# Kernel optimization log

Hardware: AMD Instinct MI355X
Metric: run time of the kernel (lower is better)

Reference implementation:

```python
import jax, jax.numpy as jnp
import numpy as np

CONF_T = 0.05
IOU_T = 0.5
K_PER_CLASS = 200  # max_detections_per_class
MAX_DET = 200      # max_detections
VAR = jnp.array([0.1, 0.1, 0.2, 0.2], jnp.float32)


def setup_inputs() -> dict:
    key = jax.random.key(0)
    k1, k2, k3, k4 = jax.random.split(key, 4)
    B, A, C = 8, 76725, 80
    # logits shifted down so most sigmoid scores fall below threshold (realistic)
    head_classifier = jax.random.normal(k1, (B, A, C), jnp.float32) - 2.0
    head_regression = jax.random.normal(k2, (B, A, 4), jnp.float32)
    centers = jax.random.uniform(k3, (A, 2), jnp.float32, 0.0, 640.0)
    sizes = jax.random.uniform(k4, (A, 2), jnp.float32, 16.0, 256.0)
    anchor_boxes = jnp.concatenate([centers, sizes], axis=-1)  # (cx, cy, w, h)
    return {"head_classifier": head_classifier,
            "head_regression": head_regression,
            "anchor_boxes": anchor_boxes}


def _decode(anchors, box_pred):
    # anchors: [1, A, 4] (cx,cy,w,h); box_pred: [B, A, 4]
    b = box_pred * VAR
    cxcy = b[..., :2] * anchors[..., 2:] + anchors[..., :2]
    wh = jnp.exp(b[..., 2:]) * anchors[..., 2:]
    # center -> corner coordinates (x1, y1, x2, y2)
    return jnp.concatenate([cxcy - wh * 0.5, cxcy + wh * 0.5], axis=-1)


def _pairwise_iou(bx):
    # bx: [K, 4] corner boxes -> [K, K] IoU
    x1, y1, x2, y2 = jnp.split(bx, 4, axis=-1)  # each [K, 1]
    area = jnp.squeeze((x2 - x1) * (y2 - y1), -1)  # [K]
    ix1 = jnp.maximum(x1, x1.T)
    iy1 = jnp.maximum(y1, y1.T)
    ix2 = jnp.minimum(x2, x2.T)
    iy2 = jnp.minimum(y2, y2.T)
    inter = jnp.clip(ix2 - ix1, 0.0) * jnp.clip(iy2 - iy1, 0.0)  # [K, K]
    union = area[:, None] + area[None, :] - inter
    return inter / jnp.maximum(union, 1e-8)


def _nms_one_class(scores, boxes):
    # scores: [A], boxes: [A, 4] -> top-K greedy NMS
    vals, idx = jax.lax.top_k(scores, K_PER_CLASS)
    b = boxes[idx]  # [K, 4]
    valid = vals > CONF_T
    iou = _pairwise_iou(b)  # [K, K]
    order = jnp.arange(K_PER_CLASS)

    def body(i, keep):
        # if box i is kept, suppress later boxes overlapping it above IOU_T
        sup = (iou[i] > IOU_T) & (order > i) & keep[i]
        return keep & ~sup

    keep = jax.lax.fori_loop(0, K_PER_CLASS, body, valid)
    return jnp.where(keep, vals, -1.0), b


def _combined(cls_scores, boxes):
    # cls_scores: [A, C], boxes: [A, 4] (shared across classes, q=1)
    sc, bx = jax.vmap(lambda s: _nms_one_class(s, boxes), in_axes=1)(cls_scores)
    C = sc.shape[0]
    cls_ids = jnp.broadcast_to(
        jnp.arange(C, dtype=jnp.float32)[:, None], (C, K_PER_CLASS))
    sc_f = sc.reshape(-1)          # [C*K]
    bx_f = bx.reshape(-1, 4)       # [C*K, 4]
    cl_f = cls_ids.reshape(-1)     # [C*K]
    top_v, top_i = jax.lax.top_k(sc_f, MAX_DET)
    ok = top_v > 0.0  # surviving detections (kept scores exceed CONF_T > 0)
    nmsed_boxes = jnp.where(ok[:, None], bx_f[top_i], 0.0)
    nmsed_scores = jnp.where(ok, top_v, 0.0)
    nmsed_classes = jnp.where(ok, cl_f[top_i], 0.0)
    valid = jnp.sum(ok).astype(jnp.int32)
    return nmsed_boxes, nmsed_scores, nmsed_classes, valid


def reference(head_classifier, head_regression, anchor_boxes):
    cls_predictions = jax.nn.sigmoid(head_classifier)          # [B, A, C]
    boxes = _decode(anchor_boxes[None, ...], head_regression)  # [B, A, 4]
    return jax.vmap(_combined)(cls_predictions, boxes)
```

## Files before the change

### kernel.cpp

```cpp
#include <hip/hip_runtime.h>
#include <cstdint>

#define TPB 256

constexpr int B_ = 8;
constexpr int A_ = 76725;
constexpr int C_ = 80;
constexpr int K_ = 200;
constexpr int S_ = 16;
constexpr int CAPS = 96;
constexpr int NBC = B_ * C_;
constexpr int P_ = 16;
constexpr int SL_ = C_ * K_ / P_;
constexpr float T0 = 0.4f;
constexpr float CONF_Tf = 0.05f;
constexpr float IOU_Tf = 0.5f;

__device__ inline uint64_t pack_key(float v, unsigned idx) {
  unsigned u = __float_as_uint(v);
  u = (u & 0x80000000u) ? ~u : (u | 0x80000000u);
  return ((uint64_t)u << 32) | (uint64_t)(0xFFFFFFFFu ^ idx);
}
__device__ inline float key_val(uint64_t k) {
  unsigned u = (unsigned)(k >> 32);
  u = (u & 0x80000000u) ? (u & 0x7FFFFFFFu) : ~u;
  return __uint_as_float(u);
}
__device__ inline unsigned key_idx(uint64_t k) { return 0xFFFFFFFFu ^ (unsigned)k; }

__device__ void radix_select(uint64_t* act, uint64_t* nxt, int n, int R,
                             uint64_t* sel, int* scnt, unsigned* hist,
                             int* s_d, int* s_ncnt) {
  int tid = threadIdx.x;
  if (tid == 0) *scnt = 0;
  __syncthreads();
  if (n <= R) {
    for (int i = tid; i < n; i += TPB) sel[i] = act[i];
    if (tid == 0) *scnt = n;
    __syncthreads();
    return;
  }
  int w = tid >> 6;
  for (int shift = 56; shift >= 0; shift -= 8) {
    for (int i = tid; i < 4 * 256; i += TPB) hist[i] = 0;
    __syncthreads();
    for (int i = tid; i < n; i += TPB)
      atomicAdd(&hist[(w << 8) + (int)((act[i] >> shift) & 255)], 1u);
    __syncthreads();
    if (tid < 256)
      hist[tid] = hist[tid] + hist[256 + tid] + hist[512 + tid] + hist[768 + tid];
    __syncthreads();
    for (int off = 1; off < 256; off <<= 1) {
      unsigned add = (tid < 256 && tid + off < 256) ? hist[tid + off] : 0u;
      __syncthreads();
      if (tid < 256) hist[tid] += add;
      __syncthreads();
    }
    if (tid < 256) {
      unsigned s = hist[tid];
      unsigned s1 = (tid == 255) ? 0u : hist[tid + 1];
      if ((int)s >= R && (int)s1 < R) *s_d = tid;
    }
    if (tid == 0) *s_ncnt = 0;
    __syncthreads();
    int d = *s_d;
    int above = (d == 255) ? 0 : (int)hist[d + 1];
    int cntd = (int)hist[d] - above;
    int need = R - above;
    if (need == cntd) {
      for (int i = tid; i < n; i += TPB)
        if ((int)((act[i] >> shift) & 255) >= d) sel[atomicAdd(scnt, 1)] = act[i];
      __syncthreads();
      return;
    }
    if (cntd == n) { R = need; continue; }
    for (int i = tid; i < n; i += TPB) {
      int dg = (int)((act[i] >> shift) & 255);
      if (dg > d) sel[atomicAdd(scnt, 1)] = act[i];
      else if (dg == d) nxt[atomicAdd(s_ncnt, 1)] = act[i];
    }
    __syncthreads();
    uint64_t* t = act; act = nxt; nxt = t;
    n = cntd; R = need;
  }
  for (int i = tid; i < R && i < n; i += TPB) sel[atomicAdd(scnt, 1)] = act[i];
  __syncthreads();
}

__device__ inline uint64_t shfl_xor_u64(uint64_t x, int m) {
  unsigned lo = (unsigned)__shfl_xor((int)(unsigned)x, m, 64);
  unsigned hi = (unsigned)__shfl_xor((int)(x >> 32), m, 64);
  return ((uint64_t)hi << 32) | lo;
}
__device__ void sort256_desc(uint64_t* sel) {
  int tid = threadIdx.x;
  uint64_t v = sel[tid];
  for (int k = 2; k <= 256; k <<= 1) {
    for (int j = k >> 1; j > 0; j >>= 1) {
      uint64_t other;
      if (j >= 64) {
        sel[tid] = v;
        __syncthreads();
        other = sel[tid ^ j];
        __syncthreads();
      } else {
        other = shfl_xor_u64(v, j);
      }
      bool up = ((tid & k) == 0);
      bool lower = ((tid & j) == 0);
      bool takeMax = (up == lower);
      bool sw = takeMax ? (other > v) : (other < v);
      v = sw ? other : v;
    }
  }
  sel[tid] = v;
  __syncthreads();
}

__device__ inline void bitonic_sort_desc_1024(uint64_t* buf, int tid) {
  for (int k = 2; k <= 1024; k <<= 1) {
    for (int j = k >> 1; j > 0; j >>= 1) {
      for (int i = tid; i < 1024; i += TPB) {
        int ixj = i ^ j;
        if (ixj > i) {
          uint64_t a = buf[i], b = buf[ixj];
          bool dir = ((i & k) == 0);
          if ((a < b) == dir) { buf[i] = b; buf[ixj] = a; }
        }
      }
      __syncthreads();
    }
  }
}
__device__ inline void compact_topk(uint64_t* buf, int* s_cnt, float* s_thr, int tid) {
  int cnt = *s_cnt;
  if (cnt > 1024) cnt = 1024;
  for (int i = cnt + tid; i < 1024; i += TPB) buf[i] = 0;
  __syncthreads();
  bitonic_sort_desc_1024(buf, tid);
  if (tid == 0) {
    *s_cnt = cnt < K_ ? cnt : K_;
    if (cnt >= K_) *s_thr = key_val(buf[K_ - 1]);
  }
  __syncthreads();
}
template <typename F>
__device__ inline void stream_topk(int n, F fetch, uint64_t* buf, int* s_cnt,
                                   float* s_thr, int tid) {
  for (int base = 0; base < n; base += TPB) {
    int i = base + tid;
    if (i < n) {
      uint64_t key; float v;
      fetch(i, key, v);
      if (v >= *s_thr) {
        int p = atomicAdd(s_cnt, 1);
        if (p < 1024) buf[p] = key;
      }
    }
    __syncthreads();
    int cur = *s_cnt;
    __syncthreads();
    if (cur >= 768) compact_topk(buf, s_cnt, s_thr, tid);
  }
  compact_topk(buf, s_cnt, s_thr, tid);
}

__global__ __launch_bounds__(TPB) void decode_kernel(const float4* __restrict__ regs,
                                                     const float4* __restrict__ anchors,
                                                     float4* __restrict__ boxes) {
  int idx = blockIdx.x * TPB + threadIdx.x;
  if (idx >= B_ * A_) return;
  int a = idx % A_;
  float4 r = regs[idx];
  float4 an = anchors[a];
  float bx = __fmul_rn(r.x, 0.1f), by = __fmul_rn(r.y, 0.1f);
  float bw = __fmul_rn(r.z, 0.2f), bh = __fmul_rn(r.w, 0.2f);
  float cx = __fadd_rn(__fmul_rn(bx, an.z), an.x);
  float cy = __fadd_rn(__fmul_rn(by, an.w), an.y);
  float w  = __fmul_rn(expf(bw), an.z);
  float h  = __fmul_rn(expf(bh), an.w);
  float hw = __fmul_rn(w, 0.5f), hh = __fmul_rn(h, 0.5f);
  boxes[idx] = make_float4(__fsub_rn(cx, hw), __fsub_rn(cy, hh),
                           __fadd_rn(cx, hw), __fadd_rn(cy, hh));
}

__global__ __launch_bounds__(TPB) void candidates_kernel(const float* __restrict__ logits,
                                                         uint64_t* __restrict__ lists,
                                                         int* __restrict__ cnts) {
  constexpr int ANCH = 256;
  constexpr int nT = (A_ + ANCH - 1) / ANCH;
  int bb = blockIdx.x / nT, t = blockIdx.x - bb * nT;
  int a0 = t * ANCH;
  int na = min(ANCH, A_ - a0);
  int bucket = blockIdx.x & (S_ - 1);
  const float4* src = (const float4*)(logits + ((size_t)bb * A_ + (size_t)a0) * C_);
  const int nq = na * (C_ / 4);
  for (int q0 = threadIdx.x; q0 < nq; q0 += TPB * 4) {
    float4 v[4];
    int qv[4] = {q0, q0 + TPB, q0 + 2 * TPB, q0 + 3 * TPB};
#pragma unroll
    for (int u = 0; u < 4; ++u)
      if (qv[u] < nq) v[u] = src[qv[u]];
#pragma unroll
    for (int u = 0; u < 4; ++u) {
      int q = qv[u];
      if (q >= nq) continue;
      float lv[4] = {v[u].x, v[u].y, v[u].z, v[u].w};
      int pos = q * 4;
      int al = pos / C_;
      int c  = pos - al * C_;
#pragma unroll
      for (int j = 0; j < 4; ++j) {
        float l = lv[j];
        if (l > T0) {
          float s = 1.0f / (1.0f + expf(-l));
          int cc = bb * C_ + c + j;
          int p = atomicAdd(&cnts[(cc * S_ + bucket) * 16], 1);
          if (p < CAPS)
            lists[((size_t)cc * S_ + bucket) * CAPS + p] = pack_key(s, (unsigned)(a0 + al));
        }
      }
    }
  }
}

__global__ __launch_bounds__(TPB) void class_nms_kernel(const float* __restrict__ logits,
                                                        const float4* __restrict__ boxes,
                                                        const uint64_t* __restrict__ lists,
                                                        const int* __restrict__ cnts,
                                                        float* __restrict__ cls_scores,
                                                        unsigned* __restrict__ cls_aidx) {
  __shared__ uint64_t s_bufA[1024];
  __shared__ uint64_t s_bufB[1024];
  __shared__ uint64_t s_sel[256];
  __shared__ unsigned s_hist[4 * 256];
  __shared__ int s_scnt, s_d, s_ncnt;
  __shared__ int s_off[S_ + 1];
  __shared__ int s_ok;
  __shared__ int s_cnt;
  __shared__ float s_thr;
  __shared__ float4 s_box[K_];
  __shared__ float s_score[K_], s_area[K_];
  __shared__ unsigned s_aidx[K_];
  __shared__ unsigned long long s_mask[K_][4];
  __shared__ unsigned long long s_keep[4];

  int tid = threadIdx.x;
  int cc = blockIdx.x;
  int bb = cc / C_, c = cc - bb * C_;

  if (tid == 0) {
    int acc = 0, ok = 1;
    for (int s = 0; s < S_; ++s) {
      int cn = cnts[(cc * S_ + s) * 16];
      if (cn > CAPS) { ok = 0; cn = CAPS; }
      s_off[s] = acc; acc += cn;
    }
    s_off[S_] = acc;
    s_ok = ok && (acc >= K_) && (acc <= 1024);
    s_cnt = 0; s_thr = CONF_Tf;
  }
  __syncthreads();
  int total = s_off[S_];
  int m;

  if (s_ok) {
    for (int s = 0; s < S_; ++s) {
      int n = s_off[s + 1] - s_off[s];
      const uint64_t* lp = lists + ((size_t)cc * S_ + s) * CAPS;
      for (int j = tid; j < n; j += TPB) s_bufA[s_off[s] + j] = lp[j];
    }
    __syncthreads();
    radix_select(s_bufA, s_bufB, total, K_, s_sel, &s_scnt, s_hist, &s_d, &s_ncnt);
    m = s_scnt;
    if (tid >= m) s_sel[tid] = 0;
    __syncthreads();
    sort256_desc(s_sel);
  } else {
    const float* col = logits + (size_t)bb * A_ * C_ + c;
    stream_topk(A_,
        [&](int i, uint64_t& key, float& v) {
          float l = col[(size_t)i * C_];
          v = 1.0f / (1.0f + expf(-l));
          key = pack_key(v, (unsigned)i);
        },
        s_bufA, &s_cnt, &s_thr, tid);
    m = s_cnt;
    s_sel[tid] = (tid < m) ? s_bufA[tid] : 0;
    __syncthreads();
  }

  if (tid < K_) {
    if (tid < m) {
      uint64_t key = s_sel[tid];
      unsigned a = key_idx(key);
      float sc = key_val(key);
      float4 bx = boxes[(size_t)bb * A_ + a];
      s_score[tid] = sc; s_aidx[tid] = a; s_box[tid] = bx;
      s_area[tid] = __fmul_rn(__fsub_rn(bx.z, bx.x), __fsub_rn(bx.w, bx.y));
    } else {
      s_score[tid] = -1.0f; s_aidx[tid] = 0u;
      s_box[tid] = make_float4(0.f, 0.f, 0.f, 0.f); s_area[tid] = 0.f;
    }
  }
  __syncthreads();

  if (tid < K_) {
    float4 bk = s_box[tid];
    float ak = s_area[tid];
    unsigned long long mw[4] = {0ull, 0ull, 0ull, 0ull};
    for (int i = 0; i < tid; ++i) {
      float4 bi = s_box[i];
      float ix1 = fmaxf(bk.x, bi.x), iy1 = fmaxf(bk.y, bi.y);
      float ix2 = fminf(bk.z, bi.z), iy2 = fminf(bk.w, bi.w);
      float iw = fmaxf(__fsub_rn(ix2, ix1), 0.f);
      float ih = fmaxf(__fsub_rn(iy2, iy1), 0.f);
      float inter = __fmul_rn(iw, ih);
      float uni = __fsub_rn(__fadd_rn(ak, s_area[i]), inter);
      float iou = inter / fmaxf(uni, 1e-8f);
      if (iou > IOU_Tf) mw[i >> 6] |= (1ull << (i & 63));
    }
    s_mask[tid][0] = mw[0]; s_mask[tid][1] = mw[1];
    s_mask[tid][2] = mw[2]; s_mask[tid][3] = mw[3];
  }
  __syncthreads();

  if (tid == 0) {
    unsigned long long k0 = 0, k1 = 0, k2 = 0, k3 = 0;
    for (int i = 0; i < m; ++i) {
      if (s_score[i] > CONF_Tf) {
        bool sup = ((s_mask[i][0] & k0) | (s_mask[i][1] & k1) |
                    (s_mask[i][2] & k2) | (s_mask[i][3] & k3)) != 0ull;
        if (!sup) {
          if (i < 64)       k0 |= 1ull << i;
          else if (i < 128) k1 |= 1ull << (i - 64);
          else if (i < 192) k2 |= 1ull << (i - 128);
          else              k3 |= 1ull << (i - 192);
        }
      }
    }
    s_keep[0] = k0; s_keep[1] = k1; s_keep[2] = k2; s_keep[3] = k3;
  }
  __syncthreads();

  if (tid < K_) {
    bool kept = (tid < m) && ((s_keep[tid >> 6] >> (tid & 63)) & 1ull);
    size_t o = (size_t)cc * K_ + tid;
    cls_scores[o] = kept ? s_score[tid] : -1.0f;
    cls_aidx[o] = s_aidx[tid];
  }
}

__global__ __launch_bounds__(TPB) void part_topk_kernel(const float* __restrict__ cls_scores,
                                                        uint64_t* __restrict__ tmp) {
  __shared__ uint64_t bufA[SL_];
  __shared__ uint64_t bufB[SL_];
  __shared__ uint64_t sel[256];
  __shared__ unsigned hist[4 * 256];
  __shared__ int s_scnt, s_d, s_ncnt;
  int tid = threadIdx.x;
  int bb = blockIdx.x / P_, part = blockIdx.x - bb * P_;
  int f0 = part * SL_;
  const float* sc = cls_scores + (size_t)bb * C_ * K_ + f0;
  for (int i = tid; i < SL_; i += TPB) bufA[i] = pack_key(sc[i], (unsigned)(f0 + i));
  __syncthreads();
  radix_select(bufA, bufB, SL_, K_, sel, &s_scnt, hist, &s_d, &s_ncnt);
  if (tid < K_) tmp[(size_t)blockIdx.x * K_ + tid] = sel[tid];
}

__global__ __launch_bounds__(TPB) void final_topk_kernel(const float4* __restrict__ boxes,
                                                         const uint64_t* __restrict__ tmp,
                                                         const unsigned* __restrict__ cls_aidx,
                                                         float* __restrict__ out) {
  constexpr int NF = P_ * K_;
  __shared__ uint64_t bufA[NF];
  __shared__ uint64_t bufB[NF];
  __shared__ uint64_t sel[256];
  __shared__ unsigned hist[4 * 256];
  __shared__ int s_scnt, s_d, s_ncnt, s_m;
  int tid = threadIdx.x;
  int bb = blockIdx.x;
  const uint64_t* tp = tmp + (size_t)bb * NF;
  for (int i = tid; i < NF; i += TPB) bufA[i] = tp[i];
  __syncthreads();
  radix_select(bufA, bufB, NF, K_, sel, &s_scnt, hist, &s_d, &s_ncnt);
  if (tid >= s_scnt) sel[tid] = 0;
  if (tid == 0) s_m = K_;
  __syncthreads();
  sort256_desc(sel);
  if (tid < K_) {
    float v = key_val(sel[tid]);
    if (!(v > 0.0f)) atomicMin(&s_m, tid);
  }
  __syncthreads();
  int m = s_m;

  if (tid < K_) {
    float4 bx = make_float4(0.f, 0.f, 0.f, 0.f);
    float sv = 0.f, cv = 0.f;
    if (tid < m) {
      uint64_t key = sel[tid];
      unsigned f = key_idx(key);
      sv = key_val(key);
      cv = (float)(f / K_);
      unsigned a = cls_aidx[(size_t)bb * C_ * K_ + f];
      bx = boxes[(size_t)bb * A_ + a];
    }
    ((float4*)out)[(size_t)bb * K_ + tid] = bx;
    out[B_ * K_ * 4 + bb * K_ + tid] = sv;
    out[B_ * K_ * 5 + bb * K_ + tid] = cv;
  }
  if (tid == 0) out[B_ * K_ * 6 + bb] = (float)m;
}

extern "C" void kernel_launch(void* const* d_in, const int* in_sizes, int n_in,
                              void* d_out, int out_size, void* d_ws, size_t ws_size,
                              hipStream_t stream) {
  const float* logits  = (const float*)d_in[0];
  const float4* regs   = (const float4*)d_in[1];
  const float4* anchors = (const float4*)d_in[2];
  float* out = (float*)d_out;

  char* ws = (char*)d_ws;
  float4* boxes     = (float4*)ws;                 size_t off = (size_t)B_ * A_ * 16;
  uint64_t* lists   = (uint64_t*)(ws + off);       off += (size_t)NBC * S_ * CAPS * 8;
  int* cnts         = (int*)(ws + off);            off += (size_t)NBC * S_ * 16 * 4;
  float* cls_scores = (float*)(ws + off);          off += (size_t)NBC * K_ * 4;
  unsigned* cls_aidx = (unsigned*)(ws + off);      off += (size_t)NBC * K_ * 4;
  uint64_t* tmp     = (uint64_t*)(ws + off);

  hipMemsetAsync(cnts, 0, (size_t)NBC * S_ * 16 * 4, stream);
  decode_kernel<<<(B_ * A_ + TPB - 1) / TPB, TPB, 0, stream>>>(regs, anchors, boxes);
  constexpr int nT = (A_ + 255) / 256;
  candidates_kernel<<<B_ * nT, TPB, 0, stream>>>(logits, lists, cnts);
  class_nms_kernel<<<NBC, TPB, 0, stream>>>(logits, boxes, lists, cnts,
                                            cls_scores, cls_aidx);
  part_topk_kernel<<<B_ * P_, TPB, 0, stream>>>(cls_scores, tmp);
  final_topk_kernel<<<B_, TPB, 0, stream>>>(boxes, tmp, cls_aidx, out);
}
```

Before: 443.5 us.

## Fuse box decode into NMS and aggregate candidates in shared memory per block

Removes the standalone decode kernel and decodes boxes only for the top-K selected anchors inside the class NMS kernel. Each class then stores its boxes directly, so the final kernel no longer gathers through anchor indices. The candidate kernel now buffers per-class hits in shared memory before one global atomic per class, and uses a single flat list of up to 1024 entries per class instead of 16 striped buckets. This cuts the full-size box workspace traffic and global atomic contention. In exchange it adds shared-memory pressure in the candidate kernel, and the unordered single list may change which overflow entries are dropped.

```diff
diff --git a/kernel.cpp b/kernel.cpp
--- a/kernel.cpp
+++ b/kernel.cpp
@@ -7,8 +7,8 @@
 constexpr int A_ = 76725;
 constexpr int C_ = 80;
 constexpr int K_ = 200;
-constexpr int S_ = 16;
-constexpr int CAPS = 96;
+constexpr int CAP = 1024;
+constexpr int LCAP = 16;
 constexpr int NBC = B_ * C_;
 constexpr int P_ = 16;
 constexpr int SL_ = C_ * K_ / P_;
@@ -165,37 +165,23 @@
   compact_topk(buf, s_cnt, s_thr, tid);
 }
 
-__global__ __launch_bounds__(TPB) void decode_kernel(const float4* __restrict__ regs,
-                                                     const float4* __restrict__ anchors,
-                                                     float4* __restrict__ boxes) {
-  int idx = blockIdx.x * TPB + threadIdx.x;
-  if (idx >= B_ * A_) return;
-  int a = idx % A_;
-  float4 r = regs[idx];
-  float4 an = anchors[a];
-  float bx = __fmul_rn(r.x, 0.1f), by = __fmul_rn(r.y, 0.1f);
-  float bw = __fmul_rn(r.z, 0.2f), bh = __fmul_rn(r.w, 0.2f);
-  float cx = __fadd_rn(__fmul_rn(bx, an.z), an.x);
-  float cy = __fadd_rn(__fmul_rn(by, an.w), an.y);
-  float w  = __fmul_rn(expf(bw), an.z);
-  float h  = __fmul_rn(expf(bh), an.w);
-  float hw = __fmul_rn(w, 0.5f), hh = __fmul_rn(h, 0.5f);
-  boxes[idx] = make_float4(__fsub_rn(cx, hw), __fsub_rn(cy, hh),
-                           __fadd_rn(cx, hw), __fadd_rn(cy, hh));
-}
-
 __global__ __launch_bounds__(TPB) void candidates_kernel(const float* __restrict__ logits,
                                                          uint64_t* __restrict__ lists,
                                                          int* __restrict__ cnts) {
+  __shared__ uint64_t s_cand[C_][LCAP];
+  __shared__ int s_cnt[C_];
   constexpr int ANCH = 256;
   constexpr int nT = (A_ + ANCH - 1) / ANCH;
   int bb = blockIdx.x / nT, t = blockIdx.x - bb * nT;
   int a0 = t * ANCH;
   int na = min(ANCH, A_ - a0);
-  int bucket = blockIdx.x & (S_ - 1);
+  int tid = threadIdx.x;
+  for (int c = tid; c < C_; c += TPB) s_cnt[c] = 0;
+  __syncthreads();
+
   const float4* src = (const float4*)(logits + ((size_t)bb * A_ + (size_t)a0) * C_);
   const int nq = na * (C_ / 4);
-  for (int q0 = threadIdx.x; q0 < nq; q0 += TPB * 4) {
+  for (int q0 = tid; q0 < nq; q0 += TPB * 4) {
     float4 v[4];
     int qv[4] = {q0, q0 + TPB, q0 + 2 * TPB, q0 + 3 * TPB};
 #pragma unroll
@@ -214,69 +200,72 @@
         float l = lv[j];
         if (l > T0) {
           float s = 1.0f / (1.0f + expf(-l));
-          int cc = bb * C_ + c + j;
-          int p = atomicAdd(&cnts[(cc * S_ + bucket) * 16], 1);
-          if (p < CAPS)
-            lists[((size_t)cc * S_ + bucket) * CAPS + p] = pack_key(s, (unsigned)(a0 + al));
+          uint64_t key = pack_key(s, (unsigned)(a0 + al));
+          int p = atomicAdd(&s_cnt[c + j], 1);
+          if (p < LCAP) {
+            s_cand[c + j][p] = key;
+          } else {
+            int cc = bb * C_ + c + j;
+            int g = atomicAdd(&cnts[cc * 16], 1);
+            if (g < CAP) lists[(size_t)cc * CAP + g] = key;
+          }
         }
       }
     }
   }
+  __syncthreads();
+
+  if (tid < C_) {
+    int n = min(s_cnt[tid], LCAP);
+    if (n > 0) {
+      int cc = bb * C_ + tid;
+      int base = atomicAdd(&cnts[cc * 16], n);
+      uint64_t* dst = lists + (size_t)cc * CAP;
+      for (int j = 0; j < n; ++j) {
+        int p = base + j;
+        if (p < CAP) dst[p] = s_cand[tid][j];
+      }
+    }
+  }
 }
 
 __global__ __launch_bounds__(TPB) void class_nms_kernel(const float* __restrict__ logits,
-                                                        const float4* __restrict__ boxes,
+                                                        const float4* __restrict__ regs,
+                                                        const float4* __restrict__ anchors,
                                                         const uint64_t* __restrict__ lists,
                                                         const int* __restrict__ cnts,
                                                         float* __restrict__ cls_scores,
-                                                        unsigned* __restrict__ cls_aidx) {
+                                                        float4* __restrict__ cls_boxes) {
   __shared__ uint64_t s_bufA[1024];
   __shared__ uint64_t s_bufB[1024];
   __shared__ uint64_t s_sel[256];
   __shared__ unsigned s_hist[4 * 256];
   __shared__ int s_scnt, s_d, s_ncnt;
-  __shared__ int s_off[S_ + 1];
-  __shared__ int s_ok;
   __shared__ int s_cnt;
   __shared__ float s_thr;
   __shared__ float4 s_box[K_];
   __shared__ float s_score[K_], s_area[K_];
-  __shared__ unsigned s_aidx[K_];
   __shared__ unsigned long long s_mask[K_][4];
   __shared__ unsigned long long s_keep[4];
 
   int tid = threadIdx.x;
   int cc = blockIdx.x;
   int bb = cc / C_, c = cc - bb * C_;
-
-  if (tid == 0) {
-    int acc = 0, ok = 1;
-    for (int s = 0; s < S_; ++s) {
-      int cn = cnts[(cc * S_ + s) * 16];
-      if (cn > CAPS) { ok = 0; cn = CAPS; }
-      s_off[s] = acc; acc += cn;
-    }
-    s_off[S_] = acc;
-    s_ok = ok && (acc >= K_) && (acc <= 1024);
-    s_cnt = 0; s_thr = CONF_Tf;
-  }
-  __syncthreads();
-  int total = s_off[S_];
+  int total = cnts[cc * 16];
   int m;
 
-  if (s_ok) {
-    for (int s = 0; s < S_; ++s) {
-      int n = s_off[s + 1] - s_off[s];
-      const uint64_t* lp = lists + ((size_t)cc * S_ + s) * CAPS;
-      for (int j = tid; j < n; j += TPB) s_bufA[s_off[s] + j] = lp[j];
-    }
+  if (total >= K_ && total <= CAP) {
+    const uint64_t* lp = lists + (size_t)cc * CAP;
+    for (int i = tid; i < total; i += TPB) s_bufA[i] = lp[i];
     __syncthreads();
     radix_select(s_bufA, s_bufB, total, K_, s_sel, &s_scnt, s_hist, &s_d, &s_ncnt);
-    m = s_scnt;
+    m = K_;
     if (tid >= m) s_sel[tid] = 0;
     __syncthreads();
     sort256_desc(s_sel);
   } else {
+    if (tid == 0) { s_cnt = 0; s_thr = CONF_Tf; }
+    __syncthreads();
     const float* col = logits + (size_t)bb * A_ * C_ + c;
     stream_topk(A_,
         [&](int i, uint64_t& key, float& v) {
@@ -294,13 +283,24 @@
     if (tid < m) {
       uint64_t key = s_sel[tid];
       unsigned a = key_idx(key);
-      float sc = key_val(key);
-      float4 bx = boxes[(size_t)bb * A_ + a];
-      s_score[tid] = sc; s_aidx[tid] = a; s_box[tid] = bx;
+      float4 r = regs[(size_t)bb * A_ + a];
+      float4 an = anchors[a];
+      float bxv = __fmul_rn(r.x, 0.1f), byv = __fmul_rn(r.y, 0.1f);
+      float bwv = __fmul_rn(r.z, 0.2f), bhv = __fmul_rn(r.w, 0.2f);
+      float cx = __fadd_rn(__fmul_rn(bxv, an.z), an.x);
+      float cy = __fadd_rn(__fmul_rn(byv, an.w), an.y);
+      float w  = __fmul_rn(expf(bwv), an.z);
+      float h  = __fmul_rn(expf(bhv), an.w);
+      float hw = __fmul_rn(w, 0.5f), hh = __fmul_rn(h, 0.5f);
+      float4 bx = make_float4(__fsub_rn(cx, hw), __fsub_rn(cy, hh),
+                              __fadd_rn(cx, hw), __fadd_rn(cy, hh));
+      s_score[tid] = key_val(key);
+      s_box[tid] = bx;
       s_area[tid] = __fmul_rn(__fsub_rn(bx.z, bx.x), __fsub_rn(bx.w, bx.y));
     } else {
-      s_score[tid] = -1.0f; s_aidx[tid] = 0u;
-      s_box[tid] = make_float4(0.f, 0.f, 0.f, 0.f); s_area[tid] = 0.f;
+      s_score[tid] = -1.0f;
+      s_box[tid] = make_float4(0.f, 0.f, 0.f, 0.f);
+      s_area[tid] = 0.f;
     }
   }
   __syncthreads();
@@ -347,7 +347,7 @@
     bool kept = (tid < m) && ((s_keep[tid >> 6] >> (tid & 63)) & 1ull);
     size_t o = (size_t)cc * K_ + tid;
     cls_scores[o] = kept ? s_score[tid] : -1.0f;
-    cls_aidx[o] = s_aidx[tid];
+    cls_boxes[o] = s_box[tid];
   }
 }
 
@@ -368,9 +368,8 @@
   if (tid < K_) tmp[(size_t)blockIdx.x * K_ + tid] = sel[tid];
 }
 
-__global__ __launch_bounds__(TPB) void final_topk_kernel(const float4* __restrict__ boxes,
+__global__ __launch_bounds__(TPB) void final_topk_kernel(const float4* __restrict__ cls_boxes,
                                                          const uint64_t* __restrict__ tmp,
-                                                         const unsigned* __restrict__ cls_aidx,
                                                          float* __restrict__ out) {
   constexpr int NF = P_ * K_;
   __shared__ uint64_t bufA[NF];
@@ -403,8 +402,7 @@
       unsigned f = key_idx(key);
       sv = key_val(key);
       cv = (float)(f / K_);
-      unsigned a = cls_aidx[(size_t)bb * C_ * K_ + f];
-      bx = boxes[(size_t)bb * A_ + a];
+      bx = cls_boxes[(size_t)bb * C_ * K_ + f];
     }
     ((float4*)out)[(size_t)bb * K_ + tid] = bx;
     out[B_ * K_ * 4 + bb * K_ + tid] = sv;
@@ -422,19 +420,17 @@
   float* out = (float*)d_out;
 
   char* ws = (char*)d_ws;
-  float4* boxes     = (float4*)ws;                 size_t off = (size_t)B_ * A_ * 16;
-  uint64_t* lists   = (uint64_t*)(ws + off);       off += (size_t)NBC * S_ * CAPS * 8;
-  int* cnts         = (int*)(ws + off);            off += (size_t)NBC * S_ * 16 * 4;
-  float* cls_scores = (float*)(ws + off);          off += (size_t)NBC * K_ * 4;
-  unsigned* cls_aidx = (unsigned*)(ws + off);      off += (size_t)NBC * K_ * 4;
-  uint64_t* tmp     = (uint64_t*)(ws + off);
-
-  hipMemsetAsync(cnts, 0, (size_t)NBC * S_ * 16 * 4, stream);
-  decode_kernel<<<(B_ * A_ + TPB - 1) / TPB, TPB, 0, stream>>>(regs, anchors, boxes);
+  uint64_t* lists    = (uint64_t*)ws;              size_t off = (size_t)NBC * CAP * 8;
+  int* cnts          = (int*)(ws + off);           off += (size_t)NBC * 16 * 4;
+  float* cls_scores  = (float*)(ws + off);         off += (size_t)NBC * K_ * 4;
+  float4* cls_boxes  = (float4*)(ws + off);        off += (size_t)NBC * K_ * 16;
+  uint64_t* tmp      = (uint64_t*)(ws + off);
+
+  hipMemsetAsync(cnts, 0, (size_t)NBC * 16 * 4, stream);
   constexpr int nT = (A_ + 255) / 256;
   candidates_kernel<<<B_ * nT, TPB, 0, stream>>>(logits, lists, cnts);
-  class_nms_kernel<<<NBC, TPB, 0, stream>>>(logits, boxes, lists, cnts,
-                                            cls_scores, cls_aidx);
+  class_nms_kernel<<<NBC, TPB, 0, stream>>>(logits, regs, anchors, lists, cnts,
+                                            cls_scores, cls_boxes);
   part_topk_kernel<<<B_ * P_, TPB, 0, stream>>>(cls_scores, tmp);
-  final_topk_kernel<<<B_, TPB, 0, stream>>>(boxes, tmp, cls_aidx, out);
-}
+  final_topk_kernel<<<B_, TPB, 0, stream>>>(cls_boxes, tmp, out);
+}
```

After: 410.2 us. 7.5% less time.
